# Performance work log

Measured on AMD Instinct MI355X. Metric: run time of the kernel, lower is better.

Reference implementation:

```python
import jax, jax.numpy as jnp
import numpy as np

N = 1_000_000
D_IN = 128
D_OUT = 128
S = 65_536


def setup_inputs() -> dict:
    key = jax.random.key(0)
    k1, k2, k3, k4 = jax.random.split(key, 4)
    element_embeddings = jax.random.normal(k1, (N, D_IN), dtype=jnp.float32)
    element_to_sample_map = jnp.sort(
        jax.random.randint(k2, (N,), 0, S, dtype=jnp.int64)
    )
    # nn.Linear(D_IN, 1, bias=False) weight -> vector [D_IN]
    w_att = jax.random.normal(k3, (D_IN,), dtype=jnp.float32) * (1.0 / np.sqrt(D_IN))
    # nn.Linear(D_IN, D_OUT, bias=False) weight [D_OUT, D_IN]
    w_out = jax.random.normal(k4, (D_OUT, D_IN), dtype=jnp.float32) * (1.0 / np.sqrt(D_IN))
    return {
        "element_embeddings": element_embeddings,
        "element_to_sample_map": element_to_sample_map,
        "num_samples": S,
        "w_att": w_att,
        "w_out": w_out,
    }


def reference(element_embeddings, element_to_sample_map, num_samples, w_att, w_out):
    seg = element_to_sample_map
    # attention scores [N]
    scores = element_embeddings @ w_att
    # segment log-softmax (numerically stable, single max/sum pass)
    seg_max = jax.ops.segment_max(scores, seg, num_segments=num_samples)
    shifted = scores - seg_max[seg]
    exp_shifted = jnp.exp(shifted)
    seg_sum = jax.ops.segment_sum(exp_shifted, seg, num_segments=num_samples)
    log_probs = shifted - jnp.log(seg_sum)[seg]
    attention_probs = jnp.exp(log_probs)  # [N]
    # output projection then weighted scatter-sum per segment -> [S, D_OUT]
    projected = element_embeddings @ w_out.T
    return jax.ops.segment_sum(
        projected * attention_probs[:, None], seg, num_segments=num_samples
    )
```

## Files before the change

### kernel.cpp

```cpp
#include <hip/hip_runtime.h>
#include <hip/hip_bf16.h>

#define N_ELEM 1000000
#define D 128
#define S_SEG 65536
#define SEGW 8
#define NBLK 2048
#define NEG_BIG (-1e30f)

__device__ __forceinline__ float halfReduce(float d) {
    #pragma unroll
    for (int off = 1; off <= 16; off <<= 1)
        d += __shfl_xor(d, off, 64);
    return d;
}

__device__ __forceinline__ float dot4(float4 v, float4 w) {
    return fmaf(v.x, w.x, fmaf(v.y, w.y, fmaf(v.z, w.z, v.w * w.w)));
}

__device__ __forceinline__ void osm_step(float& m, float& l, float4& a,
                                         float d, float4 v, bool valid) {
    float mn = valid ? fmaxf(m, d) : m;
    float scale = __expf(m - mn);
    float p = valid ? __expf(d - mn) : 0.f;
    m = mn;
    l = fmaf(l, scale, p);
    a.x = fmaf(a.x, scale, p * v.x);
    a.y = fmaf(a.y, scale, p * v.y);
    a.z = fmaf(a.z, scale, p * v.z);
    a.w = fmaf(a.w, scale, p * v.w);
}

__device__ __forceinline__ void osm_merge(float& m1, float& l1, float4& a1,
                                          float m2, float l2, float4 a2) {
    float m = fmaxf(m1, m2);
    float s1 = __expf(m1 - m), s2 = __expf(m2 - m);
    l1 = l1 * s1 + l2 * s2;
    a1.x = a1.x * s1 + a2.x * s2;
    a1.y = a1.y * s1 + a2.y * s2;
    a1.z = a1.z * s1 + a2.z * s2;
    a1.w = a1.w * s1 + a2.w * s2;
    m1 = m;
}

__global__ __launch_bounds__(256) void k_fused(
        const float* __restrict__ emb, const int* __restrict__ seg,
        const float* __restrict__ watt, float* __restrict__ out) {
    const int lane = threadIdx.x & 63;
    const int half = lane >> 5;
    const int hl   = lane & 31;
    const int wid  = blockIdx.x * 4 + (threadIdx.x >> 6);
    const float4 wv = reinterpret_cast<const float4*>(watt)[hl];
    const float4* emb4 = reinterpret_cast<const float4*>(emb);
    float4* out4 = reinterpret_cast<float4*>(out);

    const int s0 = wid * SEGW;
    int lo = 0;
    if (lane <= SEGW) {
        const int target = s0 + lane;
        int hi = N_ELEM;
        while (lo < hi) {
            int mid = (lo + hi) >> 1;
            if (seg[mid] < target) lo = mid + 1; else hi = mid;
        }
    }

    #pragma unroll 1
    for (int si = 0; si < SEGW; ++si) {
        const int beg = __shfl(lo, si, 64);
        const int end = __shfl(lo, si + 1, 64);
        float  mA = NEG_BIG, lA = 0.f; float4 aA = {0.f, 0.f, 0.f, 0.f};
        float  mB = NEG_BIG, lB = 0.f; float4 aB = {0.f, 0.f, 0.f, 0.f};
        if (beg < end) {
            float4 c0 = emb4[(size_t)min(beg + half,     N_ELEM - 1) * 32 + hl];
            float4 c1 = emb4[(size_t)min(beg + 2 + half, N_ELEM - 1) * 32 + hl];
            #pragma unroll 1
            for (int e = beg; e < end; e += 4) {
                float4 n0 = emb4[(size_t)min(e + 4 + half, N_ELEM - 1) * 32 + hl];
                float4 n1 = emb4[(size_t)min(e + 6 + half, N_ELEM - 1) * 32 + hl];
                float d0 = halfReduce(dot4(c0, wv));
                float d1 = halfReduce(dot4(c1, wv));
                osm_step(mA, lA, aA, d0, c0, (e + half)     < end);
                osm_step(mB, lB, aB, d1, c1, (e + 2 + half) < end);
                c0 = n0; c1 = n1;
            }
        }
        osm_merge(mA, lA, aA, mB, lB, aB);
        float  mo = __shfl_xor(mA, 32, 64);
        float  lo2 = __shfl_xor(lA, 32, 64);
        float4 ao;
        ao.x = __shfl_xor(aA.x, 32, 64);
        ao.y = __shfl_xor(aA.y, 32, 64);
        ao.z = __shfl_xor(aA.z, 32, 64);
        ao.w = __shfl_xor(aA.w, 32, 64);
        osm_merge(mA, lA, aA, mo, lo2, ao);
        float inv = (lA > 0.f) ? 1.0f / lA : 0.f;
        if (half == 0) {
            float4 r = {aA.x * inv, aA.y * inv, aA.z * inv, aA.w * inv};
            out4[(size_t)(s0 + si) * 32 + hl] = r;
        }
    }
}

#define PAD 132
__global__ __launch_bounds__(256) void k_proj(
        float* __restrict__ out, const float* __restrict__ wout) {
    __shared__ float As[128 * PAD];
    __shared__ float Bs[128 * PAD];
    const int tid = threadIdx.x;
    const int r0 = blockIdx.x * 128;
    for (int idx = tid; idx < 128 * 128; idx += 256) {
        int a = idx >> 7, k = idx & 127;
        As[k * PAD + a] = out[(size_t)(r0 + a) * D + k];
        Bs[k * PAD + a] = wout[(size_t)a * D + k];
    }
    __syncthreads();
    const int tx = tid & 15, ty = tid >> 4;
    const int rr = ty * 8, cc = tx * 8;
    float acc[8][8] = {};
    for (int k = 0; k < 128; ++k) {
        float a[8], b[8];
        *reinterpret_cast<float4*>(&a[0]) = *reinterpret_cast<const float4*>(&As[k * PAD + rr]);
        *reinterpret_cast<float4*>(&a[4]) = *reinterpret_cast<const float4*>(&As[k * PAD + rr + 4]);
        *reinterpret_cast<float4*>(&b[0]) = *reinterpret_cast<const float4*>(&Bs[k * PAD + cc]);
        *reinterpret_cast<float4*>(&b[4]) = *reinterpret_cast<const float4*>(&Bs[k * PAD + cc + 4]);
        #pragma unroll
        for (int i = 0; i < 8; ++i)
            #pragma unroll
            for (int j = 0; j < 8; ++j)
                acc[i][j] = fmaf(a[i], b[j], acc[i][j]);
    }
    #pragma unroll
    for (int i = 0; i < 8; ++i) {
        float4 o0 = {acc[i][0], acc[i][1], acc[i][2], acc[i][3]};
        float4 o1 = {acc[i][4], acc[i][5], acc[i][6], acc[i][7]};
        *reinterpret_cast<float4*>(&out[(size_t)(r0 + rr + i) * D + cc])     = o0;
        *reinterpret_cast<float4*>(&out[(size_t)(r0 + rr + i) * D + cc + 4]) = o1;
    }
}

extern "C" void kernel_launch(void* const* d_in, const int* in_sizes, int n_in,
                              void* d_out, int out_size, void* d_ws, size_t ws_size,
                              hipStream_t stream) {
    const float* emb  = (const float*)d_in[0];
    const int*   seg  = (const int*)d_in[1];
    const float* watt = (const float*)d_in[3];
    const float* wout = (const float*)d_in[4];
    float* out = (float*)d_out;

    k_fused<<<NBLK, 256, 0, stream>>>(emb, seg, watt, out);
    k_proj <<<S_SEG / 128, 256, 0, stream>>>(out, wout);
}
```

Measured before the change: 179.2 us.

## Split each segment across four waves with shared-memory online-softmax merge

The fused softmax-pool kernel now has the four waves of a block cooperate on the same segment. Each wave strides through a different pair of elements, and the four partial online-softmax states are merged through shared memory. Segment offsets are found once per block by binary search and stored in LDS, and four segments are processed per group with their first loads issued together. The aim is to cut per-wave serial latency on short segments and expose more memory parallelism. The cost is two block barriers per group, extra LDS traffic, and only one row in flight per half-wave instead of two.

```diff
diff --git a/kernel.cpp b/kernel.cpp
--- a/kernel.cpp
+++ b/kernel.cpp
@@ -4,8 +4,9 @@
 #define N_ELEM 1000000
 #define D 128
 #define S_SEG 65536
-#define SEGW 8
-#define NBLK 2048
+#define SEGB 32
+#define GRP 4
+#define NBLK (S_SEG / SEGB)
 #define NEG_BIG (-1e30f)
 
 __device__ __forceinline__ float halfReduce(float d) {
@@ -47,59 +48,85 @@
 __global__ __launch_bounds__(256) void k_fused(
         const float* __restrict__ emb, const int* __restrict__ seg,
         const float* __restrict__ watt, float* __restrict__ out) {
-    const int lane = threadIdx.x & 63;
+    const int tid  = threadIdx.x;
+    const int lane = tid & 63;
+    const int w    = tid >> 6;
     const int half = lane >> 5;
     const int hl   = lane & 31;
-    const int wid  = blockIdx.x * 4 + (threadIdx.x >> 6);
     const float4 wv = reinterpret_cast<const float4*>(watt)[hl];
     const float4* emb4 = reinterpret_cast<const float4*>(emb);
     float4* out4 = reinterpret_cast<float4*>(out);
 
-    const int s0 = wid * SEGW;
-    int lo = 0;
-    if (lane <= SEGW) {
-        const int target = s0 + lane;
-        int hi = N_ELEM;
+    __shared__ int    s_off[SEGB + 1];
+    __shared__ float  s_m[GRP][GRP];
+    __shared__ float  s_l[GRP][GRP];
+    __shared__ float4 s_a[GRP][GRP][32];
+
+    const int s0 = blockIdx.x * SEGB;
+    if (tid <= SEGB) {
+        int target = s0 + tid, lo = 0, hi = N_ELEM;
         while (lo < hi) {
             int mid = (lo + hi) >> 1;
             if (seg[mid] < target) lo = mid + 1; else hi = mid;
         }
+        s_off[tid] = lo;
     }
+    __syncthreads();
+
+    const float4 z4 = {0.f, 0.f, 0.f, 0.f};
 
     #pragma unroll 1
-    for (int si = 0; si < SEGW; ++si) {
-        const int beg = __shfl(lo, si, 64);
-        const int end = __shfl(lo, si + 1, 64);
-        float  mA = NEG_BIG, lA = 0.f; float4 aA = {0.f, 0.f, 0.f, 0.f};
-        float  mB = NEG_BIG, lB = 0.f; float4 aB = {0.f, 0.f, 0.f, 0.f};
-        if (beg < end) {
-            float4 c0 = emb4[(size_t)min(beg + half,     N_ELEM - 1) * 32 + hl];
-            float4 c1 = emb4[(size_t)min(beg + 2 + half, N_ELEM - 1) * 32 + hl];
+    for (int g = 0; g < SEGB / GRP; ++g) {
+        float  m[GRP], l[GRP];
+        float4 a[GRP], c[GRP];
+        int    end[GRP], e[GRP];
+        #pragma unroll
+        for (int j = 0; j < GRP; ++j) {
+            int beg = s_off[g * GRP + j];
+            end[j]  = s_off[g * GRP + j + 1];
+            m[j] = NEG_BIG; l[j] = 0.f; a[j] = z4;
+            e[j] = beg + 2 * w;
+            c[j] = emb4[(size_t)min(e[j] + half, N_ELEM - 1) * 32 + hl];
+        }
+        #pragma unroll
+        for (int j = 0; j < GRP; ++j) {
             #pragma unroll 1
-            for (int e = beg; e < end; e += 4) {
-                float4 n0 = emb4[(size_t)min(e + 4 + half, N_ELEM - 1) * 32 + hl];
-                float4 n1 = emb4[(size_t)min(e + 6 + half, N_ELEM - 1) * 32 + hl];
-                float d0 = halfReduce(dot4(c0, wv));
-                float d1 = halfReduce(dot4(c1, wv));
-                osm_step(mA, lA, aA, d0, c0, (e + half)     < end);
-                osm_step(mB, lB, aB, d1, c1, (e + 2 + half) < end);
-                c0 = n0; c1 = n1;
+            while (e[j] < end[j]) {
+                int en = e[j] + 8;
+                float4 cn = emb4[(size_t)min((en < end[j] ? en : e[j]) + half,
+                                             N_ELEM - 1) * 32 + hl];
+                float d = halfReduce(dot4(c[j], wv));
+                osm_step(m[j], l[j], a[j], d, c[j], (e[j] + half) < end[j]);
+                c[j] = cn; e[j] = en;
             }
         }
-        osm_merge(mA, lA, aA, mB, lB, aB);
-        float  mo = __shfl_xor(mA, 32, 64);
-        float  lo2 = __shfl_xor(lA, 32, 64);
-        float4 ao;
-        ao.x = __shfl_xor(aA.x, 32, 64);
-        ao.y = __shfl_xor(aA.y, 32, 64);
-        ao.z = __shfl_xor(aA.z, 32, 64);
-        ao.w = __shfl_xor(aA.w, 32, 64);
-        osm_merge(mA, lA, aA, mo, lo2, ao);
-        float inv = (lA > 0.f) ? 1.0f / lA : 0.f;
-        if (half == 0) {
-            float4 r = {aA.x * inv, aA.y * inv, aA.z * inv, aA.w * inv};
-            out4[(size_t)(s0 + si) * 32 + hl] = r;
+        #pragma unroll
+        for (int j = 0; j < GRP; ++j) {
+            float  mo = __shfl_xor(m[j], 32, 64);
+            float  lo = __shfl_xor(l[j], 32, 64);
+            float4 ao;
+            ao.x = __shfl_xor(a[j].x, 32, 64);
+            ao.y = __shfl_xor(a[j].y, 32, 64);
+            ao.z = __shfl_xor(a[j].z, 32, 64);
+            ao.w = __shfl_xor(a[j].w, 32, 64);
+            osm_merge(m[j], l[j], a[j], mo, lo, ao);
+            if (lane == 0) { s_m[w][j] = m[j]; s_l[w][j] = l[j]; }
+            if (half == 0) s_a[w][j][hl] = a[j];
         }
+        __syncthreads();
+        {
+            float  mm = s_m[0][w], ll = s_l[0][w];
+            float4 aa = s_a[0][w][hl];
+            #pragma unroll
+            for (int t = 1; t < GRP; ++t)
+                osm_merge(mm, ll, aa, s_m[t][w], s_l[t][w], s_a[t][w][hl]);
+            float inv = (ll > 0.f) ? 1.0f / ll : 0.f;
+            if (half == 0) {
+                float4 r = {aa.x * inv, aa.y * inv, aa.z * inv, aa.w * inv};
+                out4[(size_t)(s0 + g * GRP + w) * 32 + hl] = r;
+            }
+        }
+        __syncthreads();
     }
 }
 
```

After: 207.6 us. 15.8% more time.
